# Performance work log

Measured on AMD Instinct MI355X. Metric: run time of the kernel, lower is better.

Reference implementation:

```python
import jax, jax.numpy as jnp
import numpy as np
import math

EMBED_DIM = 1024
NUM_HEADS = 16
B, S = 4, 4096
NEG_INF = -1e30


def setup_inputs() -> dict:
    key = jax.random.key(0)
    k1, k2, k3, k4 = jax.random.split(key, 4)
    D = EMBED_DIM
    # xavier_uniform bounds
    lim_in = math.sqrt(6.0 / (3 * D + D))
    lim_out = math.sqrt(6.0 / (D + D))
    return {
        "x": jax.random.normal(k1, (B, S, D), dtype=jnp.float32),
        "in_proj_weight": jax.random.uniform(k2, (3 * D, D), dtype=jnp.float32, minval=-lim_in, maxval=lim_in),
        "in_proj_bias": jnp.zeros((3 * D,), dtype=jnp.float32),
        "out_proj_weight": jax.random.uniform(k3, (D, D), dtype=jnp.float32, minval=-lim_out, maxval=lim_out),
        "out_proj_bias": jnp.zeros((D,), dtype=jnp.float32),
    }


def _cron_root_attention(q, k, v):
    """Causal sqrt(N) block-sparse attention.

    q,k,v: [B, H, S, hd]. Sequence split into nb blocks of size b = sqrt(S).
    Each query attends to: (a) keys in its own block (causal within block),
    (b) one summary key per strictly-previous block (the block's last key).
    Complexity O(S * (b + nb)) = O(N * sqrt(N)).
    """
    Bq, H, Sq, hd = q.shape
    b = int(round(math.sqrt(Sq)))
    nb = Sq // b
    scale = 1.0 / math.sqrt(hd)

    qb = q.reshape(Bq, H, nb, b, hd)
    kb = k.reshape(Bq, H, nb, b, hd)
    vb = v.reshape(Bq, H, nb, b, hd)
    ks = k[:, :, b - 1::b, :]  # [B, H, nb, hd] summary keys (last of each block)
    vs = v[:, :, b - 1::b, :]

    # local (within-block) scores, causal mask
    s_loc = jnp.einsum("bhnqd,bhnkd->bhnqk", qb, kb) * scale  # [B,H,nb,b,b]
    idx = jnp.arange(b)
    loc_mask = idx[:, None] >= idx[None, :]  # [b, b]
    s_loc = jnp.where(loc_mask[None, None, None], s_loc, NEG_INF)

    # strided scores to summary keys of strictly previous blocks
    s_str = jnp.einsum("bhnqd,bhmd->bhnqm", qb, ks) * scale  # [B,H,nb,b,nb]
    nidx = jnp.arange(nb)
    str_mask = nidx[:, None] > nidx[None, :]  # [nb(query block), nb(key block)]
    s_str = jnp.where(str_mask[None, None, :, None, :], s_str, NEG_INF)

    # joint softmax over local + strided keys
    scores = jnp.concatenate([s_loc, s_str], axis=-1)  # [B,H,nb,b,b+nb]
    w = jax.nn.softmax(scores, axis=-1)
    w_loc, w_str = w[..., :b], w[..., b:]

    out = jnp.einsum("bhnqk,bhnkd->bhnqd", w_loc, vb) \
        + jnp.einsum("bhnqm,bhmd->bhnqd", w_str, vs)
    return out.reshape(Bq, H, Sq, hd)


def reference(x, in_proj_weight, in_proj_bias, out_proj_weight, out_proj_bias):
    Bx, Sx, D = x.shape
    H = NUM_HEADS
    hd = D // H
    qkv = x @ in_proj_weight.T + in_proj_bias  # [B,S,3D]
    qkv = jnp.transpose(qkv.reshape(Bx, Sx, 3, H, hd), (2, 0, 3, 1, 4))
    q, k, v = qkv[0], qkv[1], qkv[2]  # each [B,H,S,hd]
    out = _cron_root_attention(q, k, v)  # [B,H,S,hd]
    out = jnp.transpose(out, (0, 2, 1, 3)).reshape(Bx, Sx, D)
    return out @ out_proj_weight.T + out_proj_bias
```

## Files before the change

kernel.cpp:

```cpp
#include <hip/hip_runtime.h>
#include <stdint.h>

typedef __attribute__((ext_vector_type(8))) short short8;
typedef __attribute__((ext_vector_type(4))) float f32x4;
typedef __attribute__((ext_vector_type(4))) float f4;
typedef __attribute__((ext_vector_type(4))) ushort us4;

#define AS1 __attribute__((address_space(1)))
#define AS3 __attribute__((address_space(3)))

__device__ __forceinline__ ushort f2bf(float f) {
  uint u = __builtin_bit_cast(uint, f);
  u += 0x7fffu + ((u >> 16) & 1u);
  return (ushort)(u >> 16);
}

__global__ void cvt_all(const float* __restrict__ x, const float* __restrict__ wi,
                        const float* __restrict__ wo, ushort* __restrict__ xb,
                        ushort* __restrict__ wib, ushort* __restrict__ wob) {
  const int n_x = (16384 * 1024) / 4;
  const int n_wi = (3072 * 1024) / 4;
  const int n_wo = (1024 * 1024) / 4;
  const int n_tot = n_x + n_wi + n_wo;
  int i = blockIdx.x * blockDim.x + threadIdx.x;
  int stride = gridDim.x * blockDim.x;
  for (; i < n_tot; i += stride) {
    const float* src;
    ushort* dst;
    int idx;
    if (i < n_x) {
      src = x; dst = xb; idx = i;
    } else if (i < n_x + n_wi) {
      src = wi; dst = wib; idx = i - n_x;
    } else {
      src = wo; dst = wob; idx = i - n_x - n_wi;
    }
    f4 v = ((const f4*)src)[idx];
    us4 o;
    o[0] = f2bf(v[0]); o[1] = f2bf(v[1]); o[2] = f2bf(v[2]); o[3] = f2bf(v[3]);
    ((us4*)dst)[idx] = o;
  }
}


__device__ __forceinline__ void stage_half(const ushort* __restrict__ g, int pitch,
                                           int row0, int k0, char* ldsbase, int tid) {
#pragma unroll
  for (int i = 0; i < 2; ++i) {
    uint chunk = i * 512 + tid;
    uint Q = chunk << 4;
    uint L = Q ^ (((Q >> 7) & 7u) << 4);
    uint row = L >> 7;
    uint kb = L & 127u;
    const char* gp = (const char*)(g + (size_t)(row0 + (int)row) * pitch + k0) + kb;
    char* lp = ldsbase + ((i * 512 + (tid & ~63)) << 4);
    __builtin_amdgcn_global_load_lds((const AS1 void*)gp, (AS3 void*)lp, 16, 0, 0);
  }
}

__device__ __forceinline__ void stage_j(int j, const ushort* __restrict__ A,
                                        const ushort* __restrict__ Bw, int K,
                                        int arow0, int brow0, char* sA, char* sB, int tid) {
  int t = j >> 2, h = j & 3;
  int k0 = t << 6;
  char* base = ((h < 2) ? sB : sA) + ((t & 1) << 15) + ((h & 1) << 14);
  const ushort* g = (h < 2) ? Bw : A;
  int row0 = ((h < 2) ? brow0 : arow0) + ((h & 1) << 7);
  stage_half(g, K, row0, k0, base, tid);
}

template <int OUT_F32>
__global__ __launch_bounds__(512, 1) void gemm256(const ushort* __restrict__ A,
                                                  const ushort* __restrict__ Bw,
                                                  const float* __restrict__ bias,
                                                  void* __restrict__ Cout,
                                                  int M, int N, int K, int gm) {
  __shared__ char sA[65536];
  __shared__ char sB[65536];
  const int tid = threadIdx.x;
  const int lane = tid & 63, l15 = lane & 15, lk = lane >> 4;
  const int w = tid >> 6;
  const int wm = w >> 2, wn = w & 3;
  const int NT = K >> 6;

  int q8 = gridDim.x >> 3;
  int bid = blockIdx.x;
  int swz = (bid & 7) * q8 + (bid >> 3);
  int bm = swz % gm, bn = swz / gm;
  const int arow0 = bm << 8, brow0 = bn << 8;

  f32x4 acc[8][4];
  f32x4 zero = {0.f, 0.f, 0.f, 0.f};
#pragma unroll
  for (int i = 0; i < 8; ++i)
#pragma unroll
    for (int j = 0; j < 4; ++j) acc[i][j] = zero;

#pragma unroll
  for (int j = 0; j < 7; ++j) stage_j(j, A, Bw, K, arow0, brow0, sA, sB, tid);
  asm volatile("s_waitcnt vmcnt(6)" ::: "memory");
  __builtin_amdgcn_s_barrier();

  for (int t = 0; t < NT; ++t) {
    const char* bA = sA + ((t & 1) << 15);
    const char* bB = sB + ((t & 1) << 15);
    short8 bfr[4][2];
#pragma unroll
    for (int qd = 0; qd < 4; ++qd) {
      short8 afr[2][2];
      if (qd == 0) {
#pragma unroll
        for (int ni = 0; ni < 4; ++ni)
#pragma unroll
          for (int kk = 0; kk < 2; ++kk) {
            uint row = (uint)(wn * 64 + ni * 16 + l15);
            uint byte = (row << 7) + (kk << 6) + (lk << 4);
            bfr[ni][kk] = *(const short8*)&bB[byte ^ ((row & 7u) << 4)];
          }
      }
#pragma unroll
      for (int mi = 0; mi < 2; ++mi)
#pragma unroll
        for (int kk = 0; kk < 2; ++kk) {
          uint row = (uint)(wm * 128 + (qd * 2 + mi) * 16 + l15);
          uint byte = (row << 7) + (kk << 6) + (lk << 4);
          afr[mi][kk] = *(const short8*)&bA[byte ^ ((row & 7u) << 4)];
        }
      int j = 4 * t + qd + 7;
      if (j < 4 * NT) stage_j(j, A, Bw, K, arow0, brow0, sA, sB, tid);
      if (qd == 3) {
        if (t < NT - 2) asm volatile("s_waitcnt vmcnt(6)" ::: "memory");
        else if (t == NT - 2) asm volatile("s_waitcnt vmcnt(0)" ::: "memory");
      }
      __builtin_amdgcn_s_barrier();
      asm volatile("s_waitcnt lgkmcnt(0)" ::: "memory");
      __builtin_amdgcn_s_setprio(1);
#pragma unroll
      for (int kk = 0; kk < 2; ++kk)
#pragma unroll
        for (int mi = 0; mi < 2; ++mi)
#pragma unroll
          for (int ni = 0; ni < 4; ++ni)
            acc[qd * 2 + mi][ni] = __builtin_amdgcn_mfma_f32_16x16x32_bf16(
                afr[mi][kk], bfr[ni][kk], acc[qd * 2 + mi][ni], 0, 0, 0);
      __builtin_amdgcn_s_setprio(0);
      __builtin_amdgcn_s_barrier();
    }
  }

#pragma unroll
  for (int m = 0; m < 8; ++m)
#pragma unroll
    for (int ni = 0; ni < 4; ++ni)
#pragma unroll
      for (int r = 0; r < 4; ++r) {
        int row = arow0 + wm * 128 + m * 16 + lk * 4 + r;
        int col = brow0 + wn * 64 + ni * 16 + l15;
        float v = acc[m][ni][r] + bias[col];
        if constexpr (OUT_F32)
          ((float*)Cout)[(size_t)row * N + col] = v;
        else
          ((ushort*)Cout)[(size_t)row * N + col] = f2bf(v);
      }
}

__global__ __launch_bounds__(256) void cron_attn(const ushort* __restrict__ qkv,
                                                 ushort* __restrict__ aout) {
  const int S = 4096, CQ = 3072;
  int bid = blockIdx.x;
  int n = bid & 63;
  int h = (bid >> 6) & 15;
  int b = bid >> 10;
  int tid = threadIdx.x;
  int w = tid >> 6, lane = tid & 63, l15 = lane & 15, lk = lane >> 4;

  const ushort* qp = qkv + (size_t)b * S * CQ + h * 64;
  const ushort* kp = qp + 1024;
  const ushort* vp = qp + 2048;

  __shared__ char vT[16384];
  __shared__ char pL[4][4096];

  {
    int r = tid >> 1;
    int half = tid & 1;
    int srow = (r < 64) ? (n * 64 + r) : ((r - 64) * 64 + 63);
    const ushort* src = vp + (size_t)srow * CQ + half * 32;
    short8 vv0 = ((const short8*)src)[0];
    short8 vv1 = ((const short8*)src)[1];
    short8 vv2 = ((const short8*)src)[2];
    short8 vv3 = ((const short8*)src)[3];
#pragma unroll
    for (int j = 0; j < 8; ++j) {
      int d0 = half * 32 + j;
      *(short*)&vT[(uint)(d0 * 256 + r * 2) ^ (((uint)d0 & 7u) << 4)] = vv0[j];
      int d1 = half * 32 + 8 + j;
      *(short*)&vT[(uint)(d1 * 256 + r * 2) ^ (((uint)d1 & 7u) << 4)] = vv1[j];
      int d2 = half * 32 + 16 + j;
      *(short*)&vT[(uint)(d2 * 256 + r * 2) ^ (((uint)d2 & 7u) << 4)] = vv2[j];
      int d3 = half * 32 + 24 + j;
      *(short*)&vT[(uint)(d3 * 256 + r * 2) ^ (((uint)d3 & 7u) << 4)] = vv3[j];
    }
  }
  __syncthreads();

  short8 aq[2];
  {
    int srow = n * 64 + w * 16 + l15;
#pragma unroll
    for (int kk = 0; kk < 2; ++kk)
      aq[kk] = *(const short8*)(qp + (size_t)srow * CQ + kk * 32 + lk * 8);
  }

  f32x4 sc[8];
  f32x4 zero = {0.f, 0.f, 0.f, 0.f};
#pragma unroll
  for (int c = 0; c < 8; ++c) sc[c] = zero;
#pragma unroll
  for (int c = 0; c < 8; ++c) {
    int key = (c < 4) ? (n * 64 + c * 16 + l15) : (((c - 4) * 16 + l15) * 64 + 63);
    const ushort* kr = kp + (size_t)key * CQ;
#pragma unroll
    for (int kk = 0; kk < 2; ++kk) {
      short8 bk = *(const short8*)(kr + kk * 32 + lk * 8);
      sc[c] = __builtin_amdgcn_mfma_f32_16x16x32_bf16(aq[kk], bk, sc[c], 0, 0, 0);
    }
  }

  float p[8][4];
  int qrow = w * 16 + lk * 4;
#pragma unroll
  for (int c = 0; c < 8; ++c)
#pragma unroll
    for (int r = 0; r < 4; ++r) {
      float s = sc[c][r] * 0.125f;
      bool ok = (c < 4) ? ((qrow + r) >= (c * 16 + l15)) : (((c - 4) * 16 + l15) < n);
      p[c][r] = ok ? s : -1e30f;
    }

#pragma unroll
  for (int r = 0; r < 4; ++r) {
    float m = p[0][r];
#pragma unroll
    for (int c = 1; c < 8; ++c) m = fmaxf(m, p[c][r]);
    m = fmaxf(m, __shfl_xor(m, 1));
    m = fmaxf(m, __shfl_xor(m, 2));
    m = fmaxf(m, __shfl_xor(m, 4));
    m = fmaxf(m, __shfl_xor(m, 8));
    float sum = 0.f;
#pragma unroll
    for (int c = 0; c < 8; ++c) {
      p[c][r] = __expf(p[c][r] - m);
      sum += p[c][r];
    }
    sum += __shfl_xor(sum, 1);
    sum += __shfl_xor(sum, 2);
    sum += __shfl_xor(sum, 4);
    sum += __shfl_xor(sum, 8);
    float rs = 1.f / sum;
#pragma unroll
    for (int c = 0; c < 8; ++c) p[c][r] *= rs;
  }

  char* myP = pL[w];
#pragma unroll
  for (int c = 0; c < 8; ++c)
#pragma unroll
    for (int r = 0; r < 4; ++r) {
      uint row = lk * 4 + r;
      uint byte = row * 256 + (c * 16 + l15) * 2;
      *(short*)&myP[byte ^ ((row & 7u) << 4)] = (short)f2bf(p[c][r]);
    }
  short8 ap[4];
#pragma unroll
  for (int kk = 0; kk < 4; ++kk) {
    uint row = (uint)l15;
    uint byte = row * 256 + (kk * 32 + lk * 8) * 2;
    ap[kk] = *(const short8*)&myP[byte ^ ((row & 7u) << 4)];
  }

  f32x4 ao[4];
#pragma unroll
  for (int dc = 0; dc < 4; ++dc) ao[dc] = zero;
#pragma unroll
  for (int dc = 0; dc < 4; ++dc)
#pragma unroll
    for (int kk = 0; kk < 4; ++kk) {
      uint d = dc * 16 + l15;
      uint byte = d * 256 + (kk * 32 + lk * 8) * 2;
      short8 bv = *(const short8*)&vT[byte ^ ((d & 7u) << 4)];
      ao[dc] = __builtin_amdgcn_mfma_f32_16x16x32_bf16(ap[kk], bv, ao[dc], 0, 0, 0);
    }

#pragma unroll
  for (int dc = 0; dc < 4; ++dc)
#pragma unroll
    for (int r = 0; r < 4; ++r) {
      int srow = n * 64 + w * 16 + lk * 4 + r;
      int col = h * 64 + dc * 16 + l15;
      aout[((size_t)(b * S + srow)) * 1024 + col] = f2bf(ao[dc][r]);
    }
}

extern "C" void kernel_launch(void* const* d_in, const int* in_sizes, int n_in,
                              void* d_out, int out_size, void* d_ws, size_t ws_size,
                              hipStream_t stream) {
  const float* x = (const float*)d_in[0];
  const float* wi = (const float*)d_in[1];
  const float* bi = (const float*)d_in[2];
  const float* wo = (const float*)d_in[3];
  const float* bo = (const float*)d_in[4];
  float* out = (float*)d_out;
  char* ws = (char*)d_ws;

  ushort* xb = (ushort*)(ws);
  ushort* wib = (ushort*)(ws + (size_t)33554432);
  ushort* wob = (ushort*)(ws + (size_t)39845888);
  ushort* qkvb = (ushort*)(ws + (size_t)41943040);
  ushort* aob = (ushort*)(ws + (size_t)142606336);

  cvt_all<<<2048, 256, 0, stream>>>(x, wi, wo, xb, wib, wob);

  gemm256<0><<<64 * 12, 512, 0, stream>>>(xb, wib, bi, qkvb, 16384, 3072, 1024, 64);
  cron_attn<<<4096, 256, 0, stream>>>(qkvb, aob);
  gemm256<1><<<64 * 4, 512, 0, stream>>>(aob, wob, bo, out, 16384, 1024, 1024, 64);
}
```

Before: 226.3 us.

## Swap GEMM tile order, vectorize V transpose stores, raise MFMA priority

The GEMM block index mapping becomes N-fastest, so blocks on the same XCD share an activation row tile rather than a weight tile. This is meant to improve L2 reuse of the large A operand. The attention kernel's V transpose into LDS now groups four rows per thread and writes 8-byte vectors, cutting the number of LDS store instructions. s_setprio is raised around the MFMA loops to favour wavefronts that are issuing matrix ops.

```diff
diff --git a/kernel.cpp b/kernel.cpp
--- a/kernel.cpp
+++ b/kernel.cpp
@@ -2,6 +2,7 @@
 #include <stdint.h>
 
 typedef __attribute__((ext_vector_type(8))) short short8;
+typedef __attribute__((ext_vector_type(4))) short s16x4;
 typedef __attribute__((ext_vector_type(4))) float f32x4;
 typedef __attribute__((ext_vector_type(4))) float f4;
 typedef __attribute__((ext_vector_type(4))) ushort us4;
@@ -74,7 +75,7 @@
                                                   const ushort* __restrict__ Bw,
                                                   const float* __restrict__ bias,
                                                   void* __restrict__ Cout,
-                                                  int M, int N, int K, int gm) {
+                                                  int M, int N, int K, int gn) {
   __shared__ char sA[65536];
   __shared__ char sB[65536];
   const int tid = threadIdx.x;
@@ -86,7 +87,7 @@
   int q8 = gridDim.x >> 3;
   int bid = blockIdx.x;
   int swz = (bid & 7) * q8 + (bid >> 3);
-  int bm = swz % gm, bn = swz / gm;
+  int bm = swz / gn, bn = swz % gn;
   const int arow0 = bm << 8, brow0 = bn << 8;
 
   f32x4 acc[8][4];
@@ -182,24 +183,20 @@
   __shared__ char pL[4][4096];
 
   {
-    int r = tid >> 1;
-    int half = tid & 1;
-    int srow = (r < 64) ? (n * 64 + r) : ((r - 64) * 64 + 63);
-    const ushort* src = vp + (size_t)srow * CQ + half * 32;
-    short8 vv0 = ((const short8*)src)[0];
-    short8 vv1 = ((const short8*)src)[1];
-    short8 vv2 = ((const short8*)src)[2];
-    short8 vv3 = ((const short8*)src)[3];
+    int rg = tid & 31;
+    int dj = tid >> 5;
+    short8 vv[4];
+#pragma unroll
+    for (int i = 0; i < 4; ++i) {
+      int r = rg * 4 + i;
+      int srow = (r < 64) ? (n * 64 + r) : ((r - 64) * 64 + 63);
+      vv[i] = *(const short8*)(vp + (size_t)srow * CQ + dj * 8);
+    }
 #pragma unroll
     for (int j = 0; j < 8; ++j) {
-      int d0 = half * 32 + j;
-      *(short*)&vT[(uint)(d0 * 256 + r * 2) ^ (((uint)d0 & 7u) << 4)] = vv0[j];
-      int d1 = half * 32 + 8 + j;
-      *(short*)&vT[(uint)(d1 * 256 + r * 2) ^ (((uint)d1 & 7u) << 4)] = vv1[j];
-      int d2 = half * 32 + 16 + j;
-      *(short*)&vT[(uint)(d2 * 256 + r * 2) ^ (((uint)d2 & 7u) << 4)] = vv2[j];
-      int d3 = half * 32 + 24 + j;
-      *(short*)&vT[(uint)(d3 * 256 + r * 2) ^ (((uint)d3 & 7u) << 4)] = vv3[j];
+      int d = dj * 8 + j;
+      s16x4 o = {vv[0][j], vv[1][j], vv[2][j], vv[3][j]};
+      *(s16x4*)&vT[(uint)(d * 256 + rg * 8) ^ (((uint)d & 7u) << 4)] = o;
     }
   }
   __syncthreads();
@@ -216,6 +213,7 @@
   f32x4 zero = {0.f, 0.f, 0.f, 0.f};
 #pragma unroll
   for (int c = 0; c < 8; ++c) sc[c] = zero;
+  __builtin_amdgcn_s_setprio(1);
 #pragma unroll
   for (int c = 0; c < 8; ++c) {
     int key = (c < 4) ? (n * 64 + c * 16 + l15) : (((c - 4) * 16 + l15) * 64 + 63);
@@ -226,6 +224,7 @@
       sc[c] = __builtin_amdgcn_mfma_f32_16x16x32_bf16(aq[kk], bk, sc[c], 0, 0, 0);
     }
   }
+  __builtin_amdgcn_s_setprio(0);
 
   float p[8][4];
   int qrow = w * 16 + lk * 4;
@@ -282,6 +281,7 @@
   f32x4 ao[4];
 #pragma unroll
   for (int dc = 0; dc < 4; ++dc) ao[dc] = zero;
+  __builtin_amdgcn_s_setprio(1);
 #pragma unroll
   for (int dc = 0; dc < 4; ++dc)
 #pragma unroll
@@ -291,6 +291,7 @@
       short8 bv = *(const short8*)&vT[byte ^ ((d & 7u) << 4)];
       ao[dc] = __builtin_amdgcn_mfma_f32_16x16x32_bf16(ap[kk], bv, ao[dc], 0, 0, 0);
     }
+  __builtin_amdgcn_s_setprio(0);
 
 #pragma unroll
   for (int dc = 0; dc < 4; ++dc)
@@ -321,7 +322,7 @@
 
   cvt_all<<<2048, 256, 0, stream>>>(x, wi, wo, xb, wib, wob);
 
-  gemm256<0><<<64 * 12, 512, 0, stream>>>(xb, wib, bi, qkvb, 16384, 3072, 1024, 64);
+  gemm256<0><<<64 * 12, 512, 0, stream>>>(xb, wib, bi, qkvb, 16384, 3072, 1024, 12);
   cron_attn<<<4096, 256, 0, stream>>>(qkvb, aob);
-  gemm256<1><<<64 * 4, 512, 0, stream>>>(aob, wob, bo, out, 16384, 1024, 1024, 64);
-}
+  gemm256<1><<<64 * 4, 512, 0, stream>>>(aob, wob, bo, out, 16384, 1024, 1024, 4);
+}
```

Result: no change. 225.2 us (-0.5%).
